# Kernel optimization log

Hardware: AMD Instinct MI355X
Metric: run time of the kernel (lower is better)

Reference implementation:

```python
import jax, jax.numpy as jnp
import numpy as np

B, QL, ML = 8, 128, 1024
QS, KS, H = 512, 512, 256


def setup_inputs() -> dict:
    key = jax.random.key(0)
    ks = jax.random.split(key, 10)
    query = jax.random.normal(ks[0], (B, QL, QS), dtype=jnp.float32)
    memory = jax.random.normal(ks[1], (B, ML, KS), dtype=jnp.float32)
    mask = jax.random.bernoulli(ks[2], 0.1, (B, ML))
    mask = mask.at[:, 0].set(False)  # ensure at least one valid position per row
    s_q = 1.0 / np.sqrt(QS)
    s_k = 1.0 / np.sqrt(KS)
    s_h = 1.0 / np.sqrt(H)
    Wq = jax.random.uniform(ks[3], (H, QS), jnp.float32, -s_q, s_q)
    bq = jax.random.uniform(ks[4], (H,), jnp.float32, -s_q, s_q)
    Wk = jax.random.uniform(ks[5], (H, KS), jnp.float32, -s_k, s_k)
    bk = jax.random.uniform(ks[6], (H,), jnp.float32, -s_k, s_k)
    wl = jax.random.uniform(ks[7], (H,), jnp.float32, -s_h, s_h)
    bl = jax.random.uniform(ks[8], (), jnp.float32, -s_h, s_h)
    return {"query": query, "memory": memory, "mask": mask,
            "Wq": Wq, "bq": bq, "Wk": Wk, "bk": bk, "wl": wl, "bl": bl}


def reference(query, memory, mask, Wq, bq, Wk, bk, wl, bl):
    # q: [B, QL, H], k: [B, ML, H]
    q = jnp.einsum('bqs,hs->bqh', query, Wq) + bq
    k = jnp.einsum('bms,hs->bmh', memory, Wk) + bk
    # additive score: tanh(q + k) projected to scalar  -> [B, QL, ML]
    z = jnp.tanh(q[:, :, None, :] + k[:, None, :, :])  # [B, QL, ML, H]
    logits = jnp.einsum('bqmh,h->bqm', z, wl) + bl
    logits = jnp.where(mask[:, None, :], jnp.float32(-1e18), logits)
    weights = jax.nn.softmax(logits, axis=-1)  # BottleSoftmax over mem_len
    attns = jnp.einsum('bqm,bms->bqs', weights, memory)
    return attns, weights
```

## Files before the change

kernel.cpp:

```cpp
#include <hip/hip_runtime.h>

#define B_  8
#define QL_ 128
#define ML_ 1024
#define KS_ 512
#define H_  256

#define QP_OFF 0
#define KP_OFF 262144
#define MASK_OFF 2359296
#define WH_OFF 2361344
#define WL_OFF 2492416
#define MT_H_OFF 2623488
#define MT_L_OFF 4720640
#define WB_H_OFF 6817792
#define WB_L_OFF 7342080

typedef __attribute__((ext_vector_type(8))) short bfrag;
typedef __attribute__((ext_vector_type(4))) float f4acc;

__device__ __forceinline__ void split1(float v, unsigned& h, unsigned& lo) {
    unsigned u  = __float_as_uint(v);
    unsigned hb = u & 0xFFFF0000u;
    float    lf = v - __uint_as_float(hb);
    unsigned ul = __float_as_uint(lf);
    unsigned lr = ul + 0x7FFFu + ((ul >> 16) & 1u);
    h  = u >> 16;
    lo = lr >> 16;
}

__device__ __forceinline__ void split4(const float4& a, unsigned& h01, unsigned& h23,
                                       unsigned& l01, unsigned& l23) {
    unsigned h[4], l[4];
    split1(a.x, h[0], l[0]); split1(a.y, h[1], l[1]);
    split1(a.z, h[2], l[2]); split1(a.w, h[3], l[3]);
    h01 = h[0] | (h[1] << 16); h23 = h[2] | (h[3] << 16);
    l01 = l[0] | (l[1] << 16); l23 = l[2] | (l[3] << 16);
}

__global__ __launch_bounds__(256) void prep_kernel(
    const float* __restrict__ memory,
    const float* __restrict__ Wq, const float* __restrict__ Wk,
    unsigned short* __restrict__ Whi, unsigned short* __restrict__ Wlo,
    unsigned short* __restrict__ MThi, unsigned short* __restrict__ MTlo,
    const unsigned char* __restrict__ mraw, unsigned char* __restrict__ mout) {
    const int bid = blockIdx.x;
    const int t = threadIdx.x;

    if (bid == 1088) {
        __shared__ int s_not01, s_not0f;
        const unsigned int* w = (const unsigned int*)mraw;
        if (t == 0) { s_not01 = 0; s_not0f = 0; }
        __syncthreads();
        int not01 = 0, not0f = 0;
        for (int i = t; i < 2048; i += 256) {
            unsigned int v = w[i];
            if (v != 0u && v != 1u) not01 = 1;
            if (v != 0u && v != 0x3F800000u) not0f = 1;
        }
        if (not01) atomicOr(&s_not01, 1);
        if (not0f) atomicOr(&s_not0f, 1);
        __syncthreads();
        int wordTyped = (!s_not01) || (!s_not0f);
        for (int i = t; i < B_ * ML_; i += 256) {
            unsigned char mv;
            if (wordTyped) mv = (w[i] != 0u) ? 1 : 0;
            else           mv = mraw[i] ? 1 : 0;
            mout[i] = mv;
        }
        return;
    }

    if (bid < 64) {
        const float* src = (bid < 32) ? Wq : Wk;
        size_t loff = (size_t)(bid & 31) * 4096 + (size_t)t * 16;
        size_t doff = ((bid < 32) ? 0 : 131072) + loff;
        unsigned hw[8], lw[8];
#pragma unroll
        for (int i = 0; i < 4; ++i) {
            float4 v = *(const float4*)(src + loff + i * 4);
            split4(v, hw[i * 2], hw[i * 2 + 1], lw[i * 2], lw[i * 2 + 1]);
        }
        *(uint4*)(Whi + doff)     = make_uint4(hw[0], hw[1], hw[2], hw[3]);
        *(uint4*)(Whi + doff + 8) = make_uint4(hw[4], hw[5], hw[6], hw[7]);
        *(uint4*)(Wlo + doff)     = make_uint4(lw[0], lw[1], lw[2], lw[3]);
        *(uint4*)(Wlo + doff + 8) = make_uint4(lw[4], lw[5], lw[6], lw[7]);
        return;
    }

    const int idx = bid - 64;
    const int b  = idx >> 7;
    const int r  = idx & 127;
    const int mt = r >> 3;
    const int st = r & 7;
    __shared__ float T[64][68];

    const int i  = t >> 2, jb = (t & 3) << 4;
    const float* mp = memory + ((size_t)(b * ML_ + mt * 64 + i)) * KS_ + st * 64 + jb;
#pragma unroll
    for (int q = 0; q < 4; ++q)
        *(float4*)(&T[i][jb + q * 4]) = *(const float4*)(mp + q * 4);
    __syncthreads();

    const int s = t >> 2, mb = (t & 3) << 4;
    unsigned hh[16], ll[16];
#pragma unroll
    for (int e = 0; e < 16; ++e) split1(T[mb + e][s], hh[e], ll[e]);
    unsigned hp[8], lp[8];
#pragma unroll
    for (int e = 0; e < 8; ++e) {
        hp[e] = hh[2 * e] | (hh[2 * e + 1] << 16);
        lp[e] = ll[2 * e] | (ll[2 * e + 1] << 16);
    }
    const size_t doff = ((size_t)(b * KS_ + st * 64 + s)) * ML_ + mt * 64 + mb;
    *(uint4*)(MThi + doff)     = make_uint4(hp[0], hp[1], hp[2], hp[3]);
    *(uint4*)(MThi + doff + 8) = make_uint4(hp[4], hp[5], hp[6], hp[7]);
    *(uint4*)(MTlo + doff)     = make_uint4(lp[0], lp[1], lp[2], lp[3]);
    *(uint4*)(MTlo + doff + 8) = make_uint4(lp[4], lp[5], lp[6], lp[7]);
}

__global__ __launch_bounds__(256) void proj_kernel(
    const float* __restrict__ query, const float* __restrict__ memory,
    const unsigned short* __restrict__ Whi, const unsigned short* __restrict__ Wlo,
    const float* __restrict__ bq, const float* __restrict__ bk,
    float* __restrict__ Eq, float* __restrict__ Ek) {
    const int bid = blockIdx.x;
    const int t = threadIdx.x;
    const int nb = bid & 1;
    const int mb = bid >> 1;

    const float *X, *bias; float* out; int row0, wbase0;
    if (mb < 32) { X = query;  bias = bq; out = Eq; row0 = mb * 32;        wbase0 = 0; }
    else         { X = memory; bias = bk; out = Ek; row0 = (mb - 32) * 32; wbase0 = 256; }

    const int w  = t >> 6;
    const int l  = t & 63;
    const int lr = l & 15;
    const int lk = l >> 4;

    const int arow = t >> 3;
    const int acol = (t & 7) << 2;
    const float* Xp = X + (size_t)(row0 + arow) * 512 + acol;
    __shared__ unsigned int AH[2][32][16];
    __shared__ unsigned int AL[2][32][16];
    const int wg  = ((t & 7) >> 1) ^ ((arow >> 1) & 3);
    const int wwo = ((t & 7) & 1) << 1;

    const int wrow0 = wbase0 + nb * 128 + w * 32;
    const unsigned short* bhP0 = Whi + (size_t)(wrow0 + 0 * 16 + lr) * 512 + lk * 8;
    const unsigned short* bhP1 = Whi + (size_t)(wrow0 + 1 * 16 + lr) * 512 + lk * 8;
    const unsigned short* blP0 = Wlo + (size_t)(wrow0 + 0 * 16 + lr) * 512 + lk * 8;
    const unsigned short* blP1 = Wlo + (size_t)(wrow0 + 1 * 16 + lr) * 512 + lk * 8;

    f4acc acc[2][2];
#pragma unroll
    for (int mi = 0; mi < 2; ++mi)
#pragma unroll
        for (int ni = 0; ni < 2; ++ni)
            acc[mi][ni] = (f4acc){0.f, 0.f, 0.f, 0.f};

#define WRA(P, XA) do {                                               \
    unsigned h01, h23, l01, l23;                                      \
    split4(XA, h01, h23, l01, l23);                                   \
    unsigned int* dh = &AH[P][arow][wg * 4 + wwo];                    \
    unsigned int* dl = &AL[P][arow][wg * 4 + wwo];                    \
    dh[0] = h01; dh[1] = h23; dl[0] = l01; dl[1] = l23; } while (0)

#define LDB(BH0, BH1, BL0, BL1, c) do {                               \
    BH0 = *(const uint4*)(bhP0 + (size_t)(c) * 32);                   \
    BH1 = *(const uint4*)(bhP1 + (size_t)(c) * 32);                   \
    BL0 = *(const uint4*)(blP0 + (size_t)(c) * 32);                   \
    BL1 = *(const uint4*)(blP1 + (size_t)(c) * 32); } while (0)

#define COMP(P, BH0, BH1, BL0, BL1) do {                              \
    bfrag ah[2], al[2];                                               \
    _Pragma("unroll")                                                 \
    for (int mi = 0; mi < 2; ++mi) {                                  \
        int ra = mi * 16 + lr;                                        \
        int g4 = (lk ^ ((ra >> 1) & 3)) * 4;                          \
        ah[mi] = *(const bfrag*)&AH[P][ra][g4];                       \
        al[mi] = *(const bfrag*)&AL[P][ra][g4];                       \
    }                                                                 \
    bfrag bh[2], bl[2];                                               \
    bh[0] = __builtin_bit_cast(bfrag, BH0);                           \
    bh[1] = __builtin_bit_cast(bfrag, BH1);                           \
    bl[0] = __builtin_bit_cast(bfrag, BL0);                           \
    bl[1] = __builtin_bit_cast(bfrag, BL1);                           \
    _Pragma("unroll")                                                 \
    for (int mi = 0; mi < 2; ++mi)                                    \
    _Pragma("unroll")                                                 \
    for (int ni = 0; ni < 2; ++ni) {                                  \
        acc[mi][ni] = __builtin_amdgcn_mfma_f32_16x16x32_bf16(        \
            ah[mi], bh[ni], acc[mi][ni], 0, 0, 0);                    \
        acc[mi][ni] = __builtin_amdgcn_mfma_f32_16x16x32_bf16(        \
            ah[mi], bl[ni], acc[mi][ni], 0, 0, 0);                    \
        acc[mi][ni] = __builtin_amdgcn_mfma_f32_16x16x32_bf16(        \
            al[mi], bh[ni], acc[mi][ni], 0, 0, 0);                    \
    } } while (0)

    float4 xa0 = *(const float4*)(Xp);
    uint4 bh00, bh01, bl00, bl01;
    LDB(bh00, bh01, bl00, bl01, 0);
    float4 xa1 = *(const float4*)(Xp + 32);
    uint4 bh10, bh11, bl10, bl11;
    LDB(bh10, bh11, bl10, bl11, 1);
    WRA(0, xa0);
    __syncthreads();

    for (int c2 = 0; c2 < 8; ++c2) {
        WRA(1, xa1);
        if (c2 < 7) xa0 = *(const float4*)(Xp + (2 * c2 + 2) * 32);
        COMP(0, bh00, bh01, bl00, bl01);
        if (c2 < 7) LDB(bh00, bh01, bl00, bl01, 2 * c2 + 2);
        __syncthreads();
        if (c2 < 7) WRA(0, xa0);
        COMP(1, bh10, bh11, bl10, bl11);
        if (c2 < 7) {
            xa1 = *(const float4*)(Xp + (2 * c2 + 3) * 32);
            LDB(bh10, bh11, bl10, bl11, 2 * c2 + 3);
        }
        __syncthreads();
    }
#undef WRA
#undef LDB
#undef COMP

    const float SC = 2.885390081777926815f;
    float bcol[2];
#pragma unroll
    for (int ni = 0; ni < 2; ++ni) bcol[ni] = bias[nb * 128 + w * 32 + ni * 16 + lr];

#pragma unroll
    for (int mi = 0; mi < 2; ++mi)
#pragma unroll
        for (int ni = 0; ni < 2; ++ni) {
            const int col = nb * 128 + w * 32 + ni * 16 + lr;
#pragma unroll
            for (int r = 0; r < 4; ++r) {
                const int row = row0 + mi * 16 + lk * 4 + r;
                out[(size_t)row * 256 + col] =
                    __builtin_amdgcn_exp2f(SC * (acc[mi][ni][r] + bcol[ni]));
            }
        }
}

__global__ __launch_bounds__(256) void logits_kernel(
    const float* __restrict__ Eq, const float* __restrict__ Ek,
    const float* __restrict__ wl, float* __restrict__ sr) {
    const int bid = blockIdx.x;
    const int b  = bid & 7;
    const int r2 = bid >> 3;
    const int mt = r2 & 7;
    const int qt = r2 >> 3;
    const int tid = threadIdx.x;
    const int m  = tid & 127;
    const int qh = __builtin_amdgcn_readfirstlane(tid >> 7);

    __shared__ float kq[2][4][128][4];

    const float* qpb = Eq + ((size_t)(b * QL_ + qt * 8 + qh * 4)) * H_;
    const float* kpb = Ek + ((size_t)(b * ML_ + mt * 128)) * H_;

    const int srow = tid & 127;
    const int sq2  = tid >> 7;
    const float* kst = kpb + (size_t)srow * H_ + 8 * sq2;

    float4 a0 = *(const float4*)(kst);
    float4 a1 = *(const float4*)(kst + 4);
    *(float4*)(&kq[0][2 * sq2 + 0][srow][0]) = a0;
    *(float4*)(&kq[0][2 * sq2 + 1][srow][0]) = a1;
    a0 = *(const float4*)(kst + 16);
    a1 = *(const float4*)(kst + 20);
    __syncthreads();

    float acc[4] = {0.f, 0.f, 0.f, 0.f};

    for (int c = 0; c < 16; ++c) {
        const int cb = c & 1;
        if (c < 15) {
            *(float4*)(&kq[cb ^ 1][2 * sq2 + 0][srow][0]) = a0;
            *(float4*)(&kq[cb ^ 1][2 * sq2 + 1][srow][0]) = a1;
            if (c < 14) {
                a0 = *(const float4*)(kst + (c + 2) * 16);
                a1 = *(const float4*)(kst + (c + 2) * 16 + 4);
            }
        }
        const int h0 = c * 16;
#pragma unroll
        for (int quad = 0; quad < 4; ++quad) {
            float4 k4 = *(const float4*)(&kq[cb][quad][m][0]);
            float4 w4 = *(const float4*)(wl + h0 + quad * 4);
#pragma unroll
            for (int j2 = 0; j2 < 4; ++j2) {
                float4 q4 = *(const float4*)(qpb + (size_t)j2 * H_ + h0 + quad * 4);
                float p0 = fmaf(k4.x, q4.x, 1.0f);
                float p1 = fmaf(k4.y, q4.y, 1.0f);
                float p2 = fmaf(k4.z, q4.z, 1.0f);
                float p3 = fmaf(k4.w, q4.w, 1.0f);
                float p01 = p0 * p1, p23 = p2 * p3;
                float n01 = fmaf(w4.y, p0, w4.x * p1);
                float n23 = fmaf(w4.w, p2, w4.z * p3);
                float Nm  = fmaf(n23, p01, n01 * p23);
                float P   = p01 * p23;
                acc[j2] = fmaf(Nm, __builtin_amdgcn_rcpf(P), acc[j2]);
            }
        }
        __syncthreads();
    }
#pragma unroll
    for (int j2 = 0; j2 < 4; ++j2)
        sr[((size_t)(b * QL_ + qt * 8 + qh * 4 + j2)) * ML_ + mt * 128 + m] = acc[j2];
}

__global__ __launch_bounds__(256) void softmax_kernel(
    float* __restrict__ wrow_io, const unsigned char* __restrict__ mv,
    unsigned short* __restrict__ Wbhi, unsigned short* __restrict__ Wblo) {
    const int row = blockIdx.x;
    const int b = row >> 7;
    const int tid = threadIdx.x;
    float* srow = wrow_io + (size_t)row * ML_;
    const unsigned char* mrow = mv + b * ML_;
    __shared__ float red[4];

    float4 s4 = *(const float4*)(srow + tid * 4);
    uchar4 m4 = *(const uchar4*)(mrow + tid * 4);
    float l[4];
    l[0] = m4.x ? -1e18f : -2.0f * s4.x;
    l[1] = m4.y ? -1e18f : -2.0f * s4.y;
    l[2] = m4.z ? -1e18f : -2.0f * s4.z;
    l[3] = m4.w ? -1e18f : -2.0f * s4.w;

    float mx = fmaxf(fmaxf(l[0], l[1]), fmaxf(l[2], l[3]));
#pragma unroll
    for (int off = 32; off >= 1; off >>= 1)
        mx = fmaxf(mx, __shfl_xor(mx, off));
    if ((tid & 63) == 0) red[tid >> 6] = mx;
    __syncthreads();
    mx = fmaxf(fmaxf(red[0], red[1]), fmaxf(red[2], red[3]));
    __syncthreads();

    const float L2E = 1.44269504088896340736f;
    float e[4], s = 0.f;
#pragma unroll
    for (int i = 0; i < 4; ++i) {
        e[i] = __builtin_amdgcn_exp2f((l[i] - mx) * L2E);
        s += e[i];
    }
#pragma unroll
    for (int off = 32; off >= 1; off >>= 1)
        s += __shfl_xor(s, off);
    if ((tid & 63) == 0) red[tid >> 6] = s;
    __syncthreads();
    s = (red[0] + red[1]) + (red[2] + red[3]);
    float inv = __builtin_amdgcn_rcpf(s);
    float4 o = make_float4(e[0] * inv, e[1] * inv, e[2] * inv, e[3] * inv);
    *(float4*)(srow + tid * 4) = o;

    unsigned h01, h23, l01, l23;
    split4(o, h01, h23, l01, l23);
    *(uint2*)(Wbhi + (size_t)row * ML_ + tid * 4) = make_uint2(h01, h23);
    *(uint2*)(Wblo + (size_t)row * ML_ + tid * 4) = make_uint2(l01, l23);
}

__global__ __launch_bounds__(256) void attn_out_kernel(
    const unsigned short* __restrict__ Wbhi, const unsigned short* __restrict__ Wblo,
    const unsigned short* __restrict__ MThi, const unsigned short* __restrict__ MTlo,
    float* __restrict__ out) {
    const int bid = blockIdx.x;
    const int b  = bid & 7;
    const int r  = bid >> 3;
    const int mt = r & 7;
    const int nt = r >> 3;
    const int t = threadIdx.x;
    const int w  = t >> 6;
    const int l  = t & 63;
    const int lr = l & 15, lk = l >> 4;

    __shared__ unsigned short As[2][16][2][64];
    __shared__ unsigned short Bs[2][64][2][64];

    const int pa  = t >> 7;
    const int ar  = (t >> 3) & 15;
    const int acq = t & 7;
    const unsigned short* asrc = (pa ? Wblo : Wbhi)
        + ((size_t)(b * QL_ + mt * 16 + ar)) * ML_ + acq * 8;
    const int aws = (acq ^ (ar & 7)) * 8;

    const int pb  = t >> 7;
    const int br  = (t & 127) >> 1;
    const int bq0 = (t & 1) * 4;
    const unsigned short* bsrc = (pb ? MTlo : MThi)
        + ((size_t)(b * KS_ + nt * 64 + br)) * ML_ + bq0 * 8;
    int bws[4];
#pragma unroll
    for (int i2 = 0; i2 < 4; ++i2) bws[i2] = ((bq0 + i2) ^ (br & 7)) * 8;

    f4acc acc = (f4acc){0.f, 0.f, 0.f, 0.f};

    uint4 g0a, g0b0, g0b1, g0b2, g0b3;
    uint4 g1a, g1b0, g1b1, g1b2, g1b3;

#define LOADG(G, c) do {                                                  \
    G##a  = *(const uint4*)(asrc + (size_t)(c) * 64);                     \
    G##b0 = *(const uint4*)(bsrc + (size_t)(c) * 64);                     \
    G##b1 = *(const uint4*)(bsrc + (size_t)(c) * 64 + 8);                 \
    G##b2 = *(const uint4*)(bsrc + (size_t)(c) * 64 + 16);                \
    G##b3 = *(const uint4*)(bsrc + (size_t)(c) * 64 + 24); } while (0)

#define WRITEB(P, G) do {                                                 \
    *(uint4*)(&As[P][ar][pa][aws])    = G##a;                             \
    *(uint4*)(&Bs[P][br][pb][bws[0]]) = G##b0;                            \
    *(uint4*)(&Bs[P][br][pb][bws[1]]) = G##b1;                            \
    *(uint4*)(&Bs[P][br][pb][bws[2]]) = G##b2;                            \
    *(uint4*)(&Bs[P][br][pb][bws[3]]) = G##b3; } while (0)

#define COMPUTE(P) do {                                                   \
    _Pragma("unroll")                                                     \
    for (int ks = 0; ks < 2; ++ks) {                                      \
        const int k8 = (ks * 4 + lk) ^ (lr & 7);                          \
        bfrag ah = *(const bfrag*)&As[P][lr][0][k8 * 8];                  \
        bfrag al = *(const bfrag*)&As[P][lr][1][k8 * 8];                  \
        bfrag bh = *(const bfrag*)&Bs[P][w * 16 + lr][0][k8 * 8];         \
        bfrag bl = *(const bfrag*)&Bs[P][w * 16 + lr][1][k8 * 8];         \
        acc = __builtin_amdgcn_mfma_f32_16x16x32_bf16(ah, bh, acc, 0,0,0);\
        acc = __builtin_amdgcn_mfma_f32_16x16x32_bf16(ah, bl, acc, 0,0,0);\
        acc = __builtin_amdgcn_mfma_f32_16x16x32_bf16(al, bh, acc, 0,0,0);\
    } } while (0)

    LOADG(g0, 0);
    WRITEB(0, g0);
    LOADG(g1, 1);
    __syncthreads();

#pragma unroll
    for (int c = 0; c < 16; ++c) {
        if (c + 1 < 16) {
            if ((c + 1) & 1) WRITEB(1, g1); else WRITEB(0, g0);
        }
        if (c + 2 < 16) {
            if (c & 1) LOADG(g1, c + 2); else LOADG(g0, c + 2);
        }
        COMPUTE(c & 1);
        __syncthreads();
    }
#undef LOADG
#undef WRITEB
#undef COMPUTE

    const int col = nt * 64 + w * 16 + lr;
#pragma unroll
    for (int rr = 0; rr < 4; ++rr) {
        const int row = mt * 16 + lk * 4 + rr;
        out[((size_t)(b * QL_ + row)) * KS_ + col] = acc[rr];
    }
}

extern "C" void kernel_launch(void* const* d_in, const int* in_sizes, int n_in,
                              void* d_out, int out_size, void* d_ws, size_t ws_size,
                              hipStream_t stream) {
    const float* query  = (const float*)d_in[0];
    const float* memory = (const float*)d_in[1];
    const unsigned char* mask = (const unsigned char*)d_in[2];
    const float* Wq = (const float*)d_in[3];
    const float* bq = (const float*)d_in[4];
    const float* Wk = (const float*)d_in[5];
    const float* bk = (const float*)d_in[6];
    const float* wl = (const float*)d_in[7];

    float* ws = (float*)d_ws;
    float* Eq = ws + QP_OFF;
    float* Ek = ws + KP_OFF;
    unsigned char* mcan = (unsigned char*)(ws + MASK_OFF);
    unsigned short* Whi  = (unsigned short*)(ws + WH_OFF);
    unsigned short* Wlo  = (unsigned short*)(ws + WL_OFF);
    unsigned short* MThi = (unsigned short*)(ws + MT_H_OFF);
    unsigned short* MTlo = (unsigned short*)(ws + MT_L_OFF);
    unsigned short* Wbhi = (unsigned short*)(ws + WB_H_OFF);
    unsigned short* Wblo = (unsigned short*)(ws + WB_L_OFF);

    float* attns = (float*)d_out;
    float* wout  = (float*)d_out + B_ * QL_ * KS_;

    prep_kernel<<<dim3(1089), dim3(256), 0, stream>>>(memory, Wq, Wk, Whi, Wlo,
                                                      MThi, MTlo, mask, mcan);
    proj_kernel<<<dim3(576), dim3(256), 0, stream>>>(query, memory, Whi, Wlo,
                                                     bq, bk, Eq, Ek);
    logits_kernel<<<dim3(1024), dim3(256), 0, stream>>>(Eq, Ek, wl, wout);
    softmax_kernel<<<dim3(B_ * QL_), dim3(256), 0, stream>>>(wout, mcan, Wbhi, Wblo);
    attn_out_kernel<<<dim3(512), dim3(256), 0, stream>>>(Wbhi, Wblo, MThi, MTlo, attns);
}
```

Baseline: 166.0 us.

## Pre-split activations to bf16 hi/lo, retile projection GEMM, pack logits math

```diff
diff --git a/kernel.cpp b/kernel.cpp
--- a/kernel.cpp
+++ b/kernel.cpp
@@ -15,9 +15,13 @@
 #define MT_L_OFF 4720640
 #define WB_H_OFF 6817792
 #define WB_L_OFF 7342080
+#define XH_OFF 7866368
+#define XL_OFF 10225664
+#define WLP_OFF 12584960
 
 typedef __attribute__((ext_vector_type(8))) short bfrag;
 typedef __attribute__((ext_vector_type(4))) float f4acc;
+typedef __attribute__((ext_vector_type(2))) float f2;
 
 __device__ __forceinline__ void split1(float v, unsigned& h, unsigned& lo) {
     unsigned u  = __float_as_uint(v);
@@ -39,15 +43,19 @@
 }
 
 __global__ __launch_bounds__(256) void prep_kernel(
-    const float* __restrict__ memory,
+    const float* __restrict__ query, const float* __restrict__ memory,
     const float* __restrict__ Wq, const float* __restrict__ Wk,
+    const float* __restrict__ wl,
     unsigned short* __restrict__ Whi, unsigned short* __restrict__ Wlo,
+    unsigned short* __restrict__ Xhi, unsigned short* __restrict__ Xlo,
     unsigned short* __restrict__ MThi, unsigned short* __restrict__ MTlo,
-    const unsigned char* __restrict__ mraw, unsigned char* __restrict__ mout) {
+    const unsigned char* __restrict__ mraw, unsigned char* __restrict__ mout,
+    float* __restrict__ wlp) {
     const int bid = blockIdx.x;
     const int t = threadIdx.x;
 
-    if (bid == 1088) {
+    if (bid == 2240) {
+        wlp[(t & ~7) | (((t & 3) << 1) | ((t >> 2) & 1))] = wl[t];
         __shared__ int s_not01, s_not0f;
         const unsigned int* w = (const unsigned int*)mraw;
         if (t == 0) { s_not01 = 0; s_not0f = 0; }
@@ -71,182 +79,211 @@
         return;
     }
 
+    if (bid >= 1216) {
+        const int idx = bid - 1216;
+        const int b  = idx >> 7;
+        const int r  = idx & 127;
+        const int mt = r >> 3;
+        const int st = r & 7;
+        __shared__ float T[64][68];
+
+        const int i  = t >> 2, jb = (t & 3) << 4;
+        const float* mp = memory + ((size_t)(b * ML_ + mt * 64 + i)) * KS_ + st * 64 + jb;
+#pragma unroll
+        for (int q = 0; q < 4; ++q)
+            *(float4*)(&T[i][jb + q * 4]) = *(const float4*)(mp + q * 4);
+        __syncthreads();
+
+        const int s = t >> 2, mb = (t & 3) << 4;
+        unsigned hh[16], ll[16];
+#pragma unroll
+        for (int e = 0; e < 16; ++e) split1(T[mb + e][s], hh[e], ll[e]);
+        unsigned hp[8], lp[8];
+#pragma unroll
+        for (int e = 0; e < 8; ++e) {
+            hp[e] = hh[2 * e] | (hh[2 * e + 1] << 16);
+            lp[e] = ll[2 * e] | (ll[2 * e + 1] << 16);
+        }
+        const size_t doff = ((size_t)(b * KS_ + st * 64 + s)) * ML_ + mt * 64 + mb;
+        *(uint4*)(MThi + doff)     = make_uint4(hp[0], hp[1], hp[2], hp[3]);
+        *(uint4*)(MThi + doff + 8) = make_uint4(hp[4], hp[5], hp[6], hp[7]);
+        *(uint4*)(MTlo + doff)     = make_uint4(lp[0], lp[1], lp[2], lp[3]);
+        *(uint4*)(MTlo + doff + 8) = make_uint4(lp[4], lp[5], lp[6], lp[7]);
+        return;
+    }
+
+    const float* src; unsigned short *dh, *dl; size_t soff, doff;
     if (bid < 64) {
-        const float* src = (bid < 32) ? Wq : Wk;
-        size_t loff = (size_t)(bid & 31) * 4096 + (size_t)t * 16;
-        size_t doff = ((bid < 32) ? 0 : 131072) + loff;
-        unsigned hw[8], lw[8];
-#pragma unroll
-        for (int i = 0; i < 4; ++i) {
-            float4 v = *(const float4*)(src + loff + i * 4);
-            split4(v, hw[i * 2], hw[i * 2 + 1], lw[i * 2], lw[i * 2 + 1]);
-        }
-        *(uint4*)(Whi + doff)     = make_uint4(hw[0], hw[1], hw[2], hw[3]);
-        *(uint4*)(Whi + doff + 8) = make_uint4(hw[4], hw[5], hw[6], hw[7]);
-        *(uint4*)(Wlo + doff)     = make_uint4(lw[0], lw[1], lw[2], lw[3]);
-        *(uint4*)(Wlo + doff + 8) = make_uint4(lw[4], lw[5], lw[6], lw[7]);
-        return;
-    }
-
-    const int idx = bid - 64;
-    const int b  = idx >> 7;
-    const int r  = idx & 127;
-    const int mt = r >> 3;
-    const int st = r & 7;
-    __shared__ float T[64][68];
-
-    const int i  = t >> 2, jb = (t & 3) << 4;
-    const float* mp = memory + ((size_t)(b * ML_ + mt * 64 + i)) * KS_ + st * 64 + jb;
-#pragma unroll
-    for (int q = 0; q < 4; ++q)
-        *(float4*)(&T[i][jb + q * 4]) = *(const float4*)(mp + q * 4);
-    __syncthreads();
-
-    const int s = t >> 2, mb = (t & 3) << 4;
-    unsigned hh[16], ll[16];
-#pragma unroll
-    for (int e = 0; e < 16; ++e) split1(T[mb + e][s], hh[e], ll[e]);
-    unsigned hp[8], lp[8];
-#pragma unroll
-    for (int e = 0; e < 8; ++e) {
-        hp[e] = hh[2 * e] | (hh[2 * e + 1] << 16);
-        lp[e] = ll[2 * e] | (ll[2 * e + 1] << 16);
-    }
-    const size_t doff = ((size_t)(b * KS_ + st * 64 + s)) * ML_ + mt * 64 + mb;
-    *(uint4*)(MThi + doff)     = make_uint4(hp[0], hp[1], hp[2], hp[3]);
-    *(uint4*)(MThi + doff + 8) = make_uint4(hp[4], hp[5], hp[6], hp[7]);
-    *(uint4*)(MTlo + doff)     = make_uint4(lp[0], lp[1], lp[2], lp[3]);
-    *(uint4*)(MTlo + doff + 8) = make_uint4(lp[4], lp[5], lp[6], lp[7]);
+        src = (bid < 32) ? Wq : Wk;
+        soff = (size_t)(bid & 31) * 4096;
+        doff = ((bid < 32) ? 0 : 131072) + soff;
+        dh = Whi; dl = Wlo;
+    } else if (bid < 192) {
+        src = query;  soff = (size_t)(bid - 64) * 4096;  doff = soff;
+        dh = Xhi; dl = Xlo;
+    } else {
+        src = memory; soff = (size_t)(bid - 192) * 4096; doff = 524288 + soff;
+        dh = Xhi; dl = Xlo;
+    }
+    soff += (size_t)t * 16; doff += (size_t)t * 16;
+
+    unsigned hw[8], lw[8];
+#pragma unroll
+    for (int i = 0; i < 4; ++i) {
+        float4 v = *(const float4*)(src + soff + i * 4);
+        split4(v, hw[i * 2], hw[i * 2 + 1], lw[i * 2], lw[i * 2 + 1]);
+    }
+    *(uint4*)(dh + doff)     = make_uint4(hw[0], hw[1], hw[2], hw[3]);
+    *(uint4*)(dh + doff + 8) = make_uint4(hw[4], hw[5], hw[6], hw[7]);
+    *(uint4*)(dl + doff)     = make_uint4(lw[0], lw[1], lw[2], lw[3]);
+    *(uint4*)(dl + doff + 8) = make_uint4(lw[4], lw[5], lw[6], lw[7]);
 }
 
 __global__ __launch_bounds__(256) void proj_kernel(
-    const float* __restrict__ query, const float* __restrict__ memory,
+    const unsigned short* __restrict__ Xhi, const unsigned short* __restrict__ Xlo,
     const unsigned short* __restrict__ Whi, const unsigned short* __restrict__ Wlo,
     const float* __restrict__ bq, const float* __restrict__ bk,
     float* __restrict__ Eq, float* __restrict__ Ek) {
     const int bid = blockIdx.x;
     const int t = threadIdx.x;
-    const int nb = bid & 1;
-    const int mb = bid >> 1;
-
-    const float *X, *bias; float* out; int row0, wbase0;
-    if (mb < 32) { X = query;  bias = bq; out = Eq; row0 = mb * 32;        wbase0 = 0; }
-    else         { X = memory; bias = bk; out = Ek; row0 = (mb - 32) * 32; wbase0 = 256; }
+    const int wk = (bid & 7) * 144 + (bid >> 3);
+    const int nt = wk & 3;
+    const int mt = wk >> 2;
+
+    const bool isQ = (mt < 32);
+    const int arow0 = mt * 32;
+    const int orow0 = isQ ? arow0 : arow0 - 1024;
+    const float* bias = isQ ? bq : bk;
+    float* out = isQ ? Eq : Ek;
+    const int wrb = (isQ ? 0 : 256) + nt * 64;
 
     const int w  = t >> 6;
+    const int wm = w >> 1, wn = w & 1;
     const int l  = t & 63;
-    const int lr = l & 15;
-    const int lk = l >> 4;
-
-    const int arow = t >> 3;
-    const int acol = (t & 7) << 2;
-    const float* Xp = X + (size_t)(row0 + arow) * 512 + acol;
-    __shared__ unsigned int AH[2][32][16];
-    __shared__ unsigned int AL[2][32][16];
-    const int wg  = ((t & 7) >> 1) ^ ((arow >> 1) & 3);
-    const int wwo = ((t & 7) & 1) << 1;
-
-    const int wrow0 = wbase0 + nb * 128 + w * 32;
-    const unsigned short* bhP0 = Whi + (size_t)(wrow0 + 0 * 16 + lr) * 512 + lk * 8;
-    const unsigned short* bhP1 = Whi + (size_t)(wrow0 + 1 * 16 + lr) * 512 + lk * 8;
-    const unsigned short* blP0 = Wlo + (size_t)(wrow0 + 0 * 16 + lr) * 512 + lk * 8;
-    const unsigned short* blP1 = Wlo + (size_t)(wrow0 + 1 * 16 + lr) * 512 + lk * 8;
-
-    f4acc acc[2][2];
-#pragma unroll
-    for (int mi = 0; mi < 2; ++mi)
-#pragma unroll
-        for (int ni = 0; ni < 2; ++ni)
-            acc[mi][ni] = (f4acc){0.f, 0.f, 0.f, 0.f};
-
-#define WRA(P, XA) do {                                               \
-    unsigned h01, h23, l01, l23;                                      \
-    split4(XA, h01, h23, l01, l23);                                   \
-    unsigned int* dh = &AH[P][arow][wg * 4 + wwo];                    \
-    unsigned int* dl = &AL[P][arow][wg * 4 + wwo];                    \
-    dh[0] = h01; dh[1] = h23; dl[0] = l01; dl[1] = l23; } while (0)
-
-#define LDB(BH0, BH1, BL0, BL1, c) do {                               \
-    BH0 = *(const uint4*)(bhP0 + (size_t)(c) * 32);                   \
-    BH1 = *(const uint4*)(bhP1 + (size_t)(c) * 32);                   \
-    BL0 = *(const uint4*)(blP0 + (size_t)(c) * 32);                   \
-    BL1 = *(const uint4*)(blP1 + (size_t)(c) * 32); } while (0)
-
-#define COMP(P, BH0, BH1, BL0, BL1) do {                              \
-    bfrag ah[2], al[2];                                               \
-    _Pragma("unroll")                                                 \
-    for (int mi = 0; mi < 2; ++mi) {                                  \
-        int ra = mi * 16 + lr;                                        \
-        int g4 = (lk ^ ((ra >> 1) & 3)) * 4;                          \
-        ah[mi] = *(const bfrag*)&AH[P][ra][g4];                       \
-        al[mi] = *(const bfrag*)&AL[P][ra][g4];                       \
-    }                                                                 \
-    bfrag bh[2], bl[2];                                               \
-    bh[0] = __builtin_bit_cast(bfrag, BH0);                           \
-    bh[1] = __builtin_bit_cast(bfrag, BH1);                           \
-    bl[0] = __builtin_bit_cast(bfrag, BL0);                           \
-    bl[1] = __builtin_bit_cast(bfrag, BL1);                           \
-    _Pragma("unroll")                                                 \
-    for (int mi = 0; mi < 2; ++mi)                                    \
-    _Pragma("unroll")                                                 \
-    for (int ni = 0; ni < 2; ++ni) {                                  \
-        acc[mi][ni] = __builtin_amdgcn_mfma_f32_16x16x32_bf16(        \
-            ah[mi], bh[ni], acc[mi][ni], 0, 0, 0);                    \
-        acc[mi][ni] = __builtin_amdgcn_mfma_f32_16x16x32_bf16(        \
-            ah[mi], bl[ni], acc[mi][ni], 0, 0, 0);                    \
-        acc[mi][ni] = __builtin_amdgcn_mfma_f32_16x16x32_bf16(        \
-            al[mi], bh[ni], acc[mi][ni], 0, 0, 0);                    \
+    const int lr = l & 15, lk = l >> 4;
+
+    __shared__ unsigned short As[2][2][32][64];
+    __shared__ unsigned short Bs[2][2][64][64];
+
+    const int pa   = t >> 7;
+    const int slot = t & 127;
+    const int arow = slot >> 2, ao = slot & 3;
+    const int brow = slot >> 1, bo0 = (slot & 1) * 4;
+    const unsigned short* asrc = (pa ? Xlo : Xhi) + (size_t)(arow0 + arow) * 512 + ao * 8;
+    const unsigned short* bsrc = (pa ? Wlo : Whi) + (size_t)(wrb + brow) * 512 + bo0 * 8;
+    const int awd0 = (ao ^ (arow & 7)) * 8;
+    const int awd1 = ((ao + 4) ^ (arow & 7)) * 8;
+    int bwd[4];
+#pragma unroll
+    for (int i = 0; i < 4; ++i) bwd[i] = ((bo0 + i) ^ (brow & 7)) * 8;
+
+    f4acc acc[2];
+    acc[0] = (f4acc){0.f, 0.f, 0.f, 0.f};
+    acc[1] = (f4acc){0.f, 0.f, 0.f, 0.f};
+
+    uint4 g0a0, g0a1, g0b0, g0b1, g0b2, g0b3;
+    uint4 g1a0, g1a1, g1b0, g1b1, g1b2, g1b3;
+
+#define LOADG(G, c) do {                                                  \
+    G##a0 = *(const uint4*)(asrc + (size_t)(c) * 64);                     \
+    G##a1 = *(const uint4*)(asrc + (size_t)(c) * 64 + 32);                \
+    G##b0 = *(const uint4*)(bsrc + (size_t)(c) * 64);                     \
+    G##b1 = *(const uint4*)(bsrc + (size_t)(c) * 64 + 8);                 \
+    G##b2 = *(const uint4*)(bsrc + (size_t)(c) * 64 + 16);                \
+    G##b3 = *(const uint4*)(bsrc + (size_t)(c) * 64 + 24); } while (0)
+
+#define WRITEB(P, G) do {                                                 \
+    *(uint4*)(&As[P][pa][arow][awd0])  = G##a0;                           \
+    *(uint4*)(&As[P][pa][arow][awd1])  = G##a1;                           \
+    *(uint4*)(&Bs[P][pa][brow][bwd[0]]) = G##b0;                          \
+    *(uint4*)(&Bs[P][pa][brow][bwd[1]]) = G##b1;                          \
+    *(uint4*)(&Bs[P][pa][brow][bwd[2]]) = G##b2;                          \
+    *(uint4*)(&Bs[P][pa][brow][bwd[3]]) = G##b3; } while (0)
+
+#define COMPUTE(P) do {                                                   \
+    _Pragma("unroll")                                                     \
+    for (int ks = 0; ks < 2; ++ks) {                                      \
+        const int ra = wm * 16 + lr;                                      \
+        const int koA = ((ks * 4 + lk) ^ (ra & 7)) * 8;                   \
+        bfrag ah = *(const bfrag*)&As[P][0][ra][koA];                     \
+        bfrag al = *(const bfrag*)&As[P][1][ra][koA];                     \
+        _Pragma("unroll")                                                 \
+        for (int ni = 0; ni < 2; ++ni) {                                  \
+            const int rb = wn * 32 + ni * 16 + lr;                        \
+            const int koB = ((ks * 4 + lk) ^ (rb & 7)) * 8;               \
+            bfrag bh = *(const bfrag*)&Bs[P][0][rb][koB];                 \
+            bfrag bl = *(const bfrag*)&Bs[P][1][rb][koB];                 \
+            acc[ni] = __builtin_amdgcn_mfma_f32_16x16x32_bf16(            \
+                ah, bh, acc[ni], 0, 0, 0);                                \
+            acc[ni] = __builtin_amdgcn_mfma_f32_16x16x32_bf16(            \
+                ah, bl, acc[ni], 0, 0, 0);                                \
+            acc[ni] = __builtin_amdgcn_mfma_f32_16x16x32_bf16(            \
+                al, bh, acc[ni], 0, 0, 0);                                \
+        }                                                                 \
     } } while (0)
 
-    float4 xa0 = *(const float4*)(Xp);
-    uint4 bh00, bh01, bl00, bl01;
-    LDB(bh00, bh01, bl00, bl01, 0);
-    float4 xa1 = *(const float4*)(Xp + 32);
-    uint4 bh10, bh11, bl10, bl11;
-    LDB(bh10, bh11, bl10, bl11, 1);
-    WRA(0, xa0);
+    LOADG(g0, 0);
+    WRITEB(0, g0);
+    LOADG(g1, 1);
     __syncthreads();
 
-    for (int c2 = 0; c2 < 8; ++c2) {
-        WRA(1, xa1);
-        if (c2 < 7) xa0 = *(const float4*)(Xp + (2 * c2 + 2) * 32);
-        COMP(0, bh00, bh01, bl00, bl01);
-        if (c2 < 7) LDB(bh00, bh01, bl00, bl01, 2 * c2 + 2);
+#pragma unroll
+    for (int c = 0; c < 8; ++c) {
+        if (c + 1 < 8) {
+            if ((c + 1) & 1) WRITEB(1, g1); else WRITEB(0, g0);
+        }
+        if (c + 2 < 8) {
+            if (c & 1) LOADG(g1, c + 2); else LOADG(g0, c + 2);
+        }
+        COMPUTE(c & 1);
         __syncthreads();
-        if (c2 < 7) WRA(0, xa0);
-        COMP(1, bh10, bh11, bl10, bl11);
-        if (c2 < 7) {
-            xa1 = *(const float4*)(Xp + (2 * c2 + 3) * 32);
-            LDB(bh10, bh11, bl10, bl11, 2 * c2 + 3);
-        }
-        __syncthreads();
-    }
-#undef WRA
-#undef LDB
-#undef COMP
+    }
+#undef LOADG
+#undef WRITEB
+#undef COMPUTE
 
     const float SC = 2.885390081777926815f;
-    float bcol[2];
-#pragma unroll
-    for (int ni = 0; ni < 2; ++ni) bcol[ni] = bias[nb * 128 + w * 32 + ni * 16 + lr];
-
-#pragma unroll
-    for (int mi = 0; mi < 2; ++mi)
-#pragma unroll
-        for (int ni = 0; ni < 2; ++ni) {
-            const int col = nb * 128 + w * 32 + ni * 16 + lr;
-#pragma unroll
-            for (int r = 0; r < 4; ++r) {
-                const int row = row0 + mi * 16 + lk * 4 + r;
-                out[(size_t)row * 256 + col] =
-                    __builtin_amdgcn_exp2f(SC * (acc[mi][ni][r] + bcol[ni]));
-            }
-        }
+#pragma unroll
+    for (int ni = 0; ni < 2; ++ni) {
+        const int col = nt * 64 + wn * 32 + ni * 16 + lr;
+        const int colp = (col & ~7) | (((col & 3) << 1) | ((col >> 2) & 1));
+        const float bc = bias[col];
+#pragma unroll
+        for (int rr = 0; rr < 4; ++rr) {
+            const int row = orow0 + wm * 16 + lk * 4 + rr;
+            out[(size_t)row * 256 + colp] =
+                __builtin_amdgcn_exp2f(SC * (acc[ni][rr] + bc));
+        }
+    }
+}
+
+__device__ __forceinline__ f2 qterm8(const float4 k4a, const float4 k4b,
+                                     const float4 q4a, const float4 q4b,
+                                     const float4 w4a, const float4 w4b,
+                                     f2 acc) {
+    f2 kp0 = {k4a.x, k4a.y}, kp1 = {k4a.z, k4a.w};
+    f2 kp2 = {k4b.x, k4b.y}, kp3 = {k4b.z, k4b.w};
+    f2 qp0 = {q4a.x, q4a.y}, qp1 = {q4a.z, q4a.w};
+    f2 qp2 = {q4b.x, q4b.y}, qp3 = {q4b.z, q4b.w};
+    f2 wp0 = {w4a.x, w4a.y}, wp1 = {w4a.z, w4a.w};
+    f2 wp2 = {w4b.x, w4b.y}, wp3 = {w4b.z, w4b.w};
+    const f2 one2 = {1.0f, 1.0f};
+    f2 pp0 = __builtin_elementwise_fma(kp0, qp0, one2);
+    f2 pp1 = __builtin_elementwise_fma(kp1, qp1, one2);
+    f2 pp2 = __builtin_elementwise_fma(kp2, qp2, one2);
+    f2 pp3 = __builtin_elementwise_fma(kp3, qp3, one2);
+    f2 p01 = pp0 * pp1, p23 = pp2 * pp3;
+    f2 n01 = __builtin_elementwise_fma(wp1, pp0, wp0 * pp1);
+    f2 n23 = __builtin_elementwise_fma(wp3, pp2, wp2 * pp3);
+    f2 Nm  = __builtin_elementwise_fma(n23, p01, n01 * p23);
+    f2 P   = p01 * p23;
+    f2 r   = {__builtin_amdgcn_rcpf(P.x), __builtin_amdgcn_rcpf(P.y)};
+    return __builtin_elementwise_fma(Nm, r, acc);
 }
 
 __global__ __launch_bounds__(256) void logits_kernel(
     const float* __restrict__ Eq, const float* __restrict__ Ek,
-    const float* __restrict__ wl, float* __restrict__ sr) {
+    const float* __restrict__ wlp, float* __restrict__ sr) {
     const int bid = blockIdx.x;
     const int b  = bid & 7;
     const int r2 = bid >> 3;
@@ -273,7 +310,9 @@
     a1 = *(const float4*)(kst + 20);
     __syncthreads();
 
-    float acc[4] = {0.f, 0.f, 0.f, 0.f};
+    f2 accp[4];
+#pragma unroll
+    for (int j2 = 0; j2 < 4; ++j2) accp[j2] = (f2){0.f, 0.f};
 
     for (int c = 0; c < 16; ++c) {
         const int cb = c & 1;
@@ -287,29 +326,24 @@
         }
         const int h0 = c * 16;
 #pragma unroll
-        for (int quad = 0; quad < 4; ++quad) {
-            float4 k4 = *(const float4*)(&kq[cb][quad][m][0]);
-            float4 w4 = *(const float4*)(wl + h0 + quad * 4);
+        for (int pg = 0; pg < 2; ++pg) {
+            float4 k4a = *(const float4*)(&kq[cb][2 * pg + 0][m][0]);
+            float4 k4b = *(const float4*)(&kq[cb][2 * pg + 1][m][0]);
+            float4 w4a = *(const float4*)(wlp + h0 + pg * 8);
+            float4 w4b = *(const float4*)(wlp + h0 + pg * 8 + 4);
 #pragma unroll
             for (int j2 = 0; j2 < 4; ++j2) {
-                float4 q4 = *(const float4*)(qpb + (size_t)j2 * H_ + h0 + quad * 4);
-                float p0 = fmaf(k4.x, q4.x, 1.0f);
-                float p1 = fmaf(k4.y, q4.y, 1.0f);
-                float p2 = fmaf(k4.z, q4.z, 1.0f);
-                float p3 = fmaf(k4.w, q4.w, 1.0f);
-                float p01 = p0 * p1, p23 = p2 * p3;
-                float n01 = fmaf(w4.y, p0, w4.x * p1);
-                float n23 = fmaf(w4.w, p2, w4.z * p3);
-                float Nm  = fmaf(n23, p01, n01 * p23);
-                float P   = p01 * p23;
-                acc[j2] = fmaf(Nm, __builtin_amdgcn_rcpf(P), acc[j2]);
+                float4 q4a = *(const float4*)(qpb + (size_t)j2 * H_ + h0 + pg * 8);
+                float4 q4b = *(const float4*)(qpb + (size_t)j2 * H_ + h0 + pg * 8 + 4);
+                accp[j2] = qterm8(k4a, k4b, q4a, q4b, w4a, w4b, accp[j2]);
             }
         }
         __syncthreads();
     }
 #pragma unroll
     for (int j2 = 0; j2 < 4; ++j2)
-        sr[((size_t)(b * QL_ + qt * 8 + qh * 4 + j2)) * ML_ + mt * 128 + m] = acc[j2];
+        sr[((size_t)(b * QL_ + qt * 8 + qh * 4 + j2)) * ML_ + mt * 128 + m] =
+            accp[j2].x + accp[j2].y;
 }
 
 __global__ __launch_bounds__(256) void softmax_kernel(
@@ -477,15 +511,19 @@
     unsigned short* MTlo = (unsigned short*)(ws + MT_L_OFF);
     unsigned short* Wbhi = (unsigned short*)(ws + WB_H_OFF);
     unsigned short* Wblo = (unsigned short*)(ws + WB_L_OFF);
+    unsigned short* Xhi  = (unsigned short*)(ws + XH_OFF);
+    unsigned short* Xlo  = (unsigned short*)(ws + XL_OFF);
+    float* wlp = ws + WLP_OFF;
 
     float* attns = (float*)d_out;
     float* wout  = (float*)d_out + B_ * QL_ * KS_;
 
-    prep_kernel<<<dim3(1089), dim3(256), 0, stream>>>(memory, Wq, Wk, Whi, Wlo,
-                                                      MThi, MTlo, mask, mcan);
-    proj_kernel<<<dim3(576), dim3(256), 0, stream>>>(query, memory, Whi, Wlo,
-                                                     bq, bk, Eq, Ek);
-    logits_kernel<<<dim3(1024), dim3(256), 0, stream>>>(Eq, Ek, wl, wout);
+    prep_kernel<<<dim3(2241), dim3(256), 0, stream>>>(query, memory, Wq, Wk, wl,
+                                                      Whi, Wlo, Xhi, Xlo,
+                                                      MThi, MTlo, mask, mcan, wlp);
+    proj_kernel<<<dim3(1152), dim3(256), 0, stream>>>(Xhi, Xlo, Whi, Wlo,
+                                                      bq, bk, Eq, Ek);
+    logits_kernel<<<dim3(1024), dim3(256), 0, stream>>>(Eq, Ek, wlp, wout);
     softmax_kernel<<<dim3(B_ * QL_), dim3(256), 0, stream>>>(wout, mcan, Wbhi, Wblo);
     attn_out_kernel<<<dim3(512), dim3(256), 0, stream>>>(Wbhi, Wblo, MThi, MTlo, attns);
 }
```

After: 156.9 us. -5.5%, faster.
